# Kernel tuning notes

Measured on AMD Instinct MI355X. Metric: run time of the kernel, lower is better.

## Reference

```python
import jax, jax.numpy as jnp
import numpy as np

E = 512      # embed_dim
H = 8        # num_heads
D = E // H   # head_dim


def setup_inputs() -> dict:
    key = jax.random.key(0)
    ks = jax.random.split(key, 10)
    T, S, B = 2048, 2048, 4
    inp = {}
    inp["query_r"] = jax.random.normal(ks[0], (T, B, E), jnp.float32)
    inp["query_i"] = jax.random.normal(ks[1], (T, B, E), jnp.float32)
    inp["key_r"]   = jax.random.normal(ks[2], (S, B, E), jnp.float32)
    inp["key_i"]   = jax.random.normal(ks[3], (S, B, E), jnp.float32)
    inp["value_r"] = jax.random.normal(ks[4], (S, B, E), jnp.float32)
    inp["value_i"] = jax.random.normal(ks[5], (S, B, E), jnp.float32)
    # xavier-ish scale for complex weights (split real/imag)
    w_scale = 1.0 / np.sqrt(2.0 * E)
    inp["in_w_r"]  = jax.random.normal(ks[6], (3 * E, E), jnp.float32) * w_scale
    inp["in_w_i"]  = jax.random.normal(ks[7], (3 * E, E), jnp.float32) * w_scale
    inp["in_b_r"]  = jnp.zeros((3 * E,), jnp.float32)
    inp["in_b_i"]  = jnp.zeros((3 * E,), jnp.float32)
    inp["out_w_r"] = jax.random.normal(ks[8], (E, E), jnp.float32) * w_scale
    inp["out_w_i"] = jax.random.normal(ks[9], (E, E), jnp.float32) * w_scale
    inp["out_b_r"] = jnp.zeros((E,), jnp.float32)
    inp["out_b_i"] = jnp.zeros((E,), jnp.float32)
    return inp


def _clinear(xr, xi, wr, wi, br, bi):
    # complex linear: (xr + i xi) @ (wr + i wi)^T + (br + i bi)
    yr = xr @ wr.T - xi @ wi.T + br
    yi = xr @ wi.T + xi @ wr.T + bi
    return yr, yi


def reference(query_r, query_i, key_r, key_i, value_r, value_i,
              in_w_r, in_w_i, in_b_r, in_b_i,
              out_w_r, out_w_i, out_b_r, out_b_i):
    T, B, _ = query_r.shape
    S = key_r.shape[0]
    # in-projection (packed q/k/v rows of in_proj_weight)
    qr, qi = _clinear(query_r, query_i, in_w_r[:E], in_w_i[:E], in_b_r[:E], in_b_i[:E])
    kr, ki = _clinear(key_r, key_i, in_w_r[E:2*E], in_w_i[E:2*E], in_b_r[E:2*E], in_b_i[E:2*E])
    vr, vi = _clinear(value_r, value_i, in_w_r[2*E:], in_w_i[2*E:], in_b_r[2*E:], in_b_i[2*E:])
    # split heads: (T,B,E) -> (T,B,H,D)
    qr = qr.reshape(T, B, H, D); qi = qi.reshape(T, B, H, D)
    kr = kr.reshape(S, B, H, D); ki = ki.reshape(S, B, H, D)
    vr = vr.reshape(S, B, H, D); vi = vi.reshape(S, B, H, D)
    scale = 1.0 / np.sqrt(D).astype(np.float32)
    # Re[Q K^H] = Qr.Kr + Qi.Ki  (conjugate transpose cancels imag cross terms)
    scores = (jnp.einsum('tbhd,sbhd->bhts', qr, kr)
              + jnp.einsum('tbhd,sbhd->bhts', qi, ki)) * scale
    p = jax.nn.softmax(scores, axis=-1)          # (B,H,T,S) real
    # complex AV with real attention weights
    or_ = jnp.einsum('bhts,sbhd->tbhd', p, vr).reshape(T, B, E)
    oi_ = jnp.einsum('bhts,sbhd->tbhd', p, vi).reshape(T, B, E)
    # out-projection (complex linear)
    out_r, out_i = _clinear(or_, oi_, out_w_r, out_w_i, out_b_r, out_b_i)
    attn_weights = p.mean(axis=1)                # averaged over heads: (B,T,S)
    return out_r, out_i, attn_weights
```

## Files before the change

kernel.cpp:

```cpp
#include <hip/hip_runtime.h>


typedef _Float16 half8 __attribute__((ext_vector_type(8)));
typedef _Float16 half2v __attribute__((ext_vector_type(2)));
typedef float f32x4 __attribute__((ext_vector_type(4)));
typedef float f32x2 __attribute__((ext_vector_type(2)));
typedef unsigned uint2v __attribute__((ext_vector_type(2)));
typedef unsigned uint4v __attribute__((ext_vector_type(4)));

__device__ __forceinline__ f32x4 mfma16(half8 a, half8 b, f32x4 c) {
  return __builtin_amdgcn_mfma_f32_16x16x32_f16(a, b, c, 0, 0, 0);
}

__device__ __forceinline__ half8 cvt8(f32x4 a, f32x4 b) {
  half8 h;
  h[0] = (_Float16)a[0]; h[1] = (_Float16)a[1]; h[2] = (_Float16)a[2]; h[3] = (_Float16)a[3];
  h[4] = (_Float16)b[0]; h[5] = (_Float16)b[1]; h[6] = (_Float16)b[2]; h[7] = (_Float16)b[3];
  return h;
}

__device__ __forceinline__ half8 neg8(half8 a) {
  half8 r;
#pragma unroll
  for (int i = 0; i < 8; i++) r[i] = -a[i];
  return r;
}

__device__ __forceinline__ unsigned pkrtz(float a, float b) {
  return __builtin_bit_cast(unsigned, __builtin_amdgcn_cvt_pkrtz(a, b));
}

__device__ __forceinline__ float fexp2(float x) { return __builtin_amdgcn_exp2f(x); }

__device__ __forceinline__ void gload16(const void* g, void* l) {
  __builtin_amdgcn_global_load_lds((const __attribute__((address_space(1))) void*)g,
                                   (__attribute__((address_space(3))) void*)l, 16, 0, 0);
}

__global__ __launch_bounds__(256) void cvt_weights_kernel(
    const float* __restrict__ iwr, const float* __restrict__ iwi,
    const float* __restrict__ owr, const float* __restrict__ owi,
    _Float16* __restrict__ dst) {
  const int i = blockIdx.x * 256 + threadIdx.x;
  const float* src;
  long so, doff;
  if (i < 98304)       { src = iwr; so = (long)i * 8;            doff = so; }
  else if (i < 196608) { src = iwi; so = (long)(i - 98304) * 8;  doff = 786432 + so; }
  else if (i < 229376) { src = owr; so = (long)(i - 196608) * 8; doff = 1572864 + so; }
  else                 { src = owi; so = (long)(i - 229376) * 8; doff = 1835008 + so; }
  f32x4 a = *(const f32x4*)(src + so);
  f32x4 b = *(const f32x4*)(src + so + 4);
  *(half8*)(dst + doff) = cvt8(a, b);
}

__global__ __launch_bounds__(256, 2) void inproj_kernel(
    const float* __restrict__ xqr, const float* __restrict__ xqi,
    const float* __restrict__ xkr, const float* __restrict__ xki,
    const float* __restrict__ xvr, const float* __restrict__ xvi,
    const _Float16* __restrict__ wr, const _Float16* __restrict__ wi,
    const float* __restrict__ br_, const float* __restrict__ bi_,
    _Float16* __restrict__ qp, _Float16* __restrict__ kp,
    _Float16* __restrict__ vp) {
  __shared__ float As_r[4096], As_i[4096];
  __shared__ _Float16 Bs_r[4096], Bs_i[4096];
  const int proj = blockIdx.z;
  const float* xr = (proj == 0) ? xqr : (proj == 1) ? xkr : xvr;
  const float* xi = (proj == 0) ? xqi : (proj == 1) ? xki : xvi;
  const int lane = threadIdx.x & 63, wave = threadIdx.x >> 6;
  const int c = lane & 15, g = lane >> 4;
  const int wrow = (wave >> 1) * 64, wcol = (wave & 1) * 64;
  const int m0 = blockIdx.x * 128, n0 = blockIdx.y * 128;

  const int acol = ((lane & 7) ^ (lane >> 3)) * 4;
  const int bcol = ((lane & 3) ^ ((lane >> 3) & 3)) * 8;
  const int sa = (c & 7) << 2;
  const int sb = ((c >> 1) & 3) << 3;

  f32x4 accR[4][4] = {};
  f32x4 accI[4][4] = {};

#pragma unroll 1
  for (int kk = 0; kk < 512; kk += 32) {
#pragma unroll
    for (int q = 0; q < 4; q++) {
      const int grp = wave * 4 + q;
      const int arow = grp * 8 + (lane >> 3);
      const long go = (long)(m0 + arow) * 512 + kk + acol;
      gload16(xr + go, &As_r[grp * 256]);
      gload16(xi + go, &As_i[grp * 256]);
    }
#pragma unroll
    for (int q = 0; q < 2; q++) {
      const int grp = wave * 2 + q;
      const int brow = grp * 16 + (lane >> 2);
      const long go = (long)(proj * 512 + n0 + brow) * 512 + kk + bcol;
      gload16(wr + go, &Bs_r[grp * 512]);
      gload16(wi + go, &Bs_i[grp * 512]);
    }
    __syncthreads();
    half8 a_r[4], a_i[4], a_ni[4];
#pragma unroll
    for (int mt = 0; mt < 4; mt++) {
      const int arow = wrow + mt * 16 + c;
      f32x4 lo = *(const f32x4*)&As_r[arow * 32 + ((g * 8) ^ sa)];
      f32x4 hi = *(const f32x4*)&As_r[arow * 32 + ((g * 8 + 4) ^ sa)];
      a_r[mt] = cvt8(lo, hi);
      lo = *(const f32x4*)&As_i[arow * 32 + ((g * 8) ^ sa)];
      hi = *(const f32x4*)&As_i[arow * 32 + ((g * 8 + 4) ^ sa)];
      a_i[mt] = cvt8(lo, hi);
      a_ni[mt] = neg8(a_i[mt]);
    }
#pragma unroll
    for (int nt = 0; nt < 4; nt++) {
      const int brow = wcol + nt * 16 + c;
      const half8 bR = *(const half8*)&Bs_r[brow * 32 + ((g * 8) ^ sb)];
      const half8 bI = *(const half8*)&Bs_i[brow * 32 + ((g * 8) ^ sb)];
#pragma unroll
      for (int mt = 0; mt < 4; mt++) {
        accR[mt][nt] = mfma16(a_r[mt], bR, accR[mt][nt]);
        accR[mt][nt] = mfma16(a_ni[mt], bI, accR[mt][nt]);
        accI[mt][nt] = mfma16(a_r[mt], bI, accI[mt][nt]);
        accI[mt][nt] = mfma16(a_i[mt], bR, accI[mt][nt]);
      }
    }
    __syncthreads();
  }
#pragma unroll
  for (int nt = 0; nt < 4; nt++) {
    const int n = n0 + wcol + nt * 16 + c;
    const float vbr = br_[proj * 512 + n];
    const float vbi = bi_[proj * 512 + n];
    const int hh = n >> 6, dl = n & 63;
#pragma unroll
    for (int mt = 0; mt < 4; mt++)
#pragma unroll
      for (int r = 0; r < 4; r++) {
        const int m = m0 + wrow + mt * 16 + g * 4 + r;
        const float yr = accR[mt][nt][r] + vbr;
        const float yi = accI[mt][nt][r] + vbi;
        const int row = m >> 2, bb = m & 3;
        if (proj == 2) {
          const long o = ((long)((bb * 8 + hh) * 64 + (row >> 5)) << 12)
                       + ((long)(dl >> 4) << 10)
                       + ((((row >> 3) & 3) * 16 + (dl & 15)) * 8) + (row & 7);
          vp[o] = (_Float16)yr;
          vp[o + 512] = (_Float16)yi;
        } else {
          const long o = ((long)((bb * 8 + hh) * 128 + (row >> 4)) << 11)
                       + ((long)(dl >> 5) << 10)
                       + ((((dl >> 3) & 3) * 16 + (row & 15)) * 8) + (dl & 7);
          _Float16* dst = (proj == 0) ? qp : kp;
          dst[o] = (_Float16)yr;
          dst[o + 512] = (_Float16)yi;
        }
      }
  }
}

__device__ __forceinline__ void p1_load(half8 (&a)[8],
    const _Float16* kb, int s0) {
  const _Float16* p = kb + (long)(s0 >> 4) * 2048;
#pragma unroll
  for (int j = 0; j < 4; j++) {
    a[j]     = *(const half8*)(p + j * 512);
    a[4 + j] = *(const half8*)(p + 2048 + j * 512);
  }
}

__device__ __forceinline__ void p1_proc(const half8 (&a)[8], const half8 (&qf)[4],
                                        float& mrun, float& lrun) {
  const float SC2 = 0.18033688011112042f;
  f32x4 acc0 = {0.f, 0.f, 0.f, 0.f}, acc1 = {0.f, 0.f, 0.f, 0.f};
  __builtin_amdgcn_s_setprio(1);
  acc0 = mfma16(a[0], qf[0], acc0);
  acc0 = mfma16(a[1], qf[1], acc0);
  acc0 = mfma16(a[2], qf[2], acc0);
  acc0 = mfma16(a[3], qf[3], acc0);
  acc1 = mfma16(a[4], qf[0], acc1);
  acc1 = mfma16(a[5], qf[1], acc1);
  acc1 = mfma16(a[6], qf[2], acc1);
  acc1 = mfma16(a[7], qf[3], acc1);
  __builtin_amdgcn_s_setprio(0);
  float s2[8];
#pragma unroll
  for (int r = 0; r < 4; r++) { s2[r] = acc0[r] * SC2; s2[4 + r] = acc1[r] * SC2; }
  float tm = s2[0];
#pragma unroll
  for (int j = 1; j < 8; j++) tm = fmaxf(tm, s2[j]);
  const float nm = fmaxf(mrun, tm);
  float sum = 0.0f;
#pragma unroll
  for (int j = 0; j < 8; j++) sum += fexp2(s2[j] - nm);
  lrun = lrun * fexp2(mrun - nm) + sum;
  mrun = nm;
}

__global__ __launch_bounds__(256) void pass1_kernel(
    const _Float16* __restrict__ qp, const _Float16* __restrict__ kp,
    float* __restrict__ c_out) {
  const int lane = threadIdx.x & 63, wave = threadIdx.x >> 6;
  const int c = lane & 15;
  const int lin = blockIdx.x;
  const int h = lin & 7, b = (lin >> 3) & 3;
  const int t0 = (lin >> 5) * 64 + wave * 16;

  const _Float16* qb = qp + ((long)(b * 8 + h) * 128 + (t0 >> 4)) * 2048 + lane * 8;
  half8 qf[4];
#pragma unroll
  for (int j = 0; j < 4; j++) qf[j] = *(const half8*)(qb + j * 512);

  float mrun = -1e30f, lrun = 0.0f;
  const _Float16* kb = kp + (long)(b * 8 + h) * 262144 + lane * 8;

  half8 bufA[8], bufB[8];
  p1_load(bufA, kb, 0);
  p1_load(bufB, kb, 32);
#pragma unroll 1
  for (int s0 = 0; s0 < 2048; s0 += 64) {
    p1_proc(bufA, qf, mrun, lrun);
    p1_load(bufA, kb, (s0 + 64) & 2047);
    p1_proc(bufB, qf, mrun, lrun);
    p1_load(bufB, kb, (s0 + 96) & 2047);
  }
#pragma unroll
  for (int off = 16; off <= 32; off <<= 1) {
    const float mo = __shfl_xor(mrun, off, 64);
    const float lo = __shfl_xor(lrun, off, 64);
    const float nm = fmaxf(mrun, mo);
    lrun = lrun * fexp2(mrun - nm) + lo * fexp2(mo - nm);
    mrun = nm;
  }
  if (lane < 16) {
    const int idx = (b * 8 + h) * 2048 + t0 + c;
    c_out[idx] = -(mrun + __log2f(lrun));
  }
}

__device__ __forceinline__ void load_kswap(half8 (&kf)[8],
    const _Float16* kb, int s) {
  const _Float16* p = kb + (long)(s >> 4) * 2048;
#pragma unroll
  for (int j = 0; j < 4; j++) {
    kf[j]     = *(const half8*)(p + j * 512);
    kf[4 + j] = *(const half8*)(p + 2048 + j * 512);
  }
}

__device__ __forceinline__ void load_vv(half8 (&vf)[8],
    const _Float16* vb, int s) {
  const _Float16* p = vb + (long)(s >> 5) * 4096;
#pragma unroll
  for (int t = 0; t < 8; t++) vf[t] = *(const half8*)(p + t * 512);
}

__device__ __forceinline__ void p2_compute(
    int s0, _Float16* wbuf, half8 (&kf)[8], half8 (&vf)[8],
    const half8 (&qf)[8], float c0, float c1,
    f32x4 (&oacc)[2][4][2],
    const _Float16* kb, const _Float16* vb,
    int c, int g, int h) {
  const float SC2 = 0.18033688011112042f;
  f32x4 sacc[2][2];
  __builtin_amdgcn_s_setprio(1);
#pragma unroll
  for (int st = 0; st < 2; st++)
#pragma unroll
    for (int sq = 0; sq < 2; sq++) {
      f32x4 a = {0.f, 0.f, 0.f, 0.f};
      a = mfma16(kf[sq * 4 + 0], qf[st * 4 + 0], a);
      a = mfma16(kf[sq * 4 + 1], qf[st * 4 + 1], a);
      a = mfma16(kf[sq * 4 + 2], qf[st * 4 + 2], a);
      a = mfma16(kf[sq * 4 + 3], qf[st * 4 + 3], a);
      sacc[st][sq] = a;
    }
  __builtin_amdgcn_s_setprio(0);
  const int sn = (s0 + 32) & 2047;
  load_kswap(kf, kb, sn);
  half8 pa0, pa1;
#pragma unroll
  for (int st = 0; st < 2; st++) {
    const float cc = st ? c1 : c0;
    float p[8];
#pragma unroll
    for (int r = 0; r < 4; r++) {
      p[r]     = fexp2(fmaf(sacc[st][0][r], SC2, cc));
      p[4 + r] = fexp2(fmaf(sacc[st][1][r], SC2, cc));
    }
    const unsigned X0 = pkrtz(p[0], p[1]), X1 = pkrtz(p[2], p[3]);
    const unsigned Y0 = pkrtz(p[4], p[5]), Y1 = pkrtz(p[6], p[7]);
    const uint2v ab0 = __builtin_amdgcn_permlane32_swap(X0, Y0, false, false);
    const uint2v ab1 = __builtin_amdgcn_permlane32_swap(X1, Y1, false, false);
    const uint2v cd0 = __builtin_amdgcn_permlane16_swap(ab0[0], ab0[1], false, false);
    const uint2v cd1 = __builtin_amdgcn_permlane16_swap(ab1[0], ab1[1], false, false);
    uint4v u;
    u[0] = cd0[0]; u[1] = cd1[0]; u[2] = cd0[1]; u[3] = cd1[1];
    const half8 pav = __builtin_bit_cast(half8, u);
    if (st == 0) pa0 = pav; else pa1 = pav;
    *(half8*)(wbuf + (h * 32 + st * 16 + c) * 40 + g * 8) = pav;
  }
  __builtin_amdgcn_s_setprio(1);
#pragma unroll
  for (int dt = 0; dt < 4; dt++) {
    oacc[0][dt][0] = mfma16(pa0, vf[dt * 2 + 0], oacc[0][dt][0]);
    oacc[0][dt][1] = mfma16(pa0, vf[dt * 2 + 1], oacc[0][dt][1]);
    oacc[1][dt][0] = mfma16(pa1, vf[dt * 2 + 0], oacc[1][dt][0]);
    oacc[1][dt][1] = mfma16(pa1, vf[dt * 2 + 1], oacc[1][dt][1]);
  }
  __builtin_amdgcn_s_setprio(0);
  load_vv(vf, vb, sn);
}

__device__ __forceinline__ void p2_meanread(
    const _Float16* rbuf, int s_read, float* attn_base, int tid) {
  const _Float16* mp = rbuf + (tid >> 4) * 40 + (tid & 15) * 2;
  half2v s = *(const half2v*)(mp);
#pragma unroll
  for (int w = 1; w < 8; w++) s += *(const half2v*)(mp + w * 1280);
  f32x2 out2 = {(float)s[0] * 0.125f, (float)s[1] * 0.125f};
  *(f32x2*)(attn_base + s_read) = out2;
}

__global__ __launch_bounds__(512, 2) void pass2_kernel(
    const _Float16* __restrict__ qp, const _Float16* __restrict__ kp,
    const _Float16* __restrict__ vp,
    const float* __restrict__ c_in,
    _Float16* __restrict__ orh, _Float16* __restrict__ oih,
    float* __restrict__ attn) {
  __shared__ _Float16 plds[4][8][32][40];
  const int tid = threadIdx.x;
  const int lane = tid & 63, h = tid >> 6;
  const int c = lane & 15, g = lane >> 4;
  const int lin = blockIdx.x;
  const int b = (lin & 7) >> 1;
  const int t0 = (((lin & 1) << 5) | (lin >> 3)) * 32;

  const _Float16* qb = qp + ((long)(b * 8 + h) * 128 + (t0 >> 4)) * 2048 + lane * 8;
  half8 qf[8];
#pragma unroll
  for (int st = 0; st < 2; st++)
#pragma unroll
    for (int j = 0; j < 4; j++)
      qf[st * 4 + j] = *(const half8*)(qb + st * 2048 + j * 512);

  const int midx = (b * 8 + h) * 2048 + t0 + c;
  const float c0 = c_in[midx];
  const float c1 = c_in[midx + 16];

  f32x4 oacc[2][4][2] = {};
  const _Float16* kb = kp + (long)(b * 8 + h) * 262144 + lane * 8;
  const _Float16* vb = vp + (long)(b * 8 + h) * 262144 + lane * 8;
  float* attn_base = attn + ((long)b * 2048 + t0 + (tid >> 4)) * 2048 + (tid & 15) * 2;
  _Float16* pb0 = &plds[0][0][0][0];
  _Float16* pb1 = &plds[1][0][0][0];
  _Float16* pb2 = &plds[2][0][0][0];
  _Float16* pb3 = &plds[3][0][0][0];

  half8 kf[8], vf[8];
  load_kswap(kf, kb, 0);
  load_vv(vf, vb, 0);

#pragma unroll 1
  for (int s0 = 0; s0 < 2048; s0 += 128) {
    p2_compute(s0, pb0, kf, vf, qf, c0, c1, oacc, kb, vb, c, g, h);
    __syncthreads();
    if (s0 >= 32) p2_meanread(pb3, s0 - 32, attn_base, tid);
    p2_compute(s0 + 32, pb1, kf, vf, qf, c0, c1, oacc, kb, vb, c, g, h);
    __syncthreads();
    p2_meanread(pb0, s0, attn_base, tid);
    p2_compute(s0 + 64, pb2, kf, vf, qf, c0, c1, oacc, kb, vb, c, g, h);
    __syncthreads();
    p2_meanread(pb1, s0 + 32, attn_base, tid);
    p2_compute(s0 + 96, pb3, kf, vf, qf, c0, c1, oacc, kb, vb, c, g, h);
    __syncthreads();
    p2_meanread(pb2, s0 + 64, attn_base, tid);
  }
  p2_meanread(pb3, 2016, attn_base, tid);

#pragma unroll
  for (int st = 0; st < 2; st++)
#pragma unroll
    for (int dt = 0; dt < 4; dt++)
#pragma unroll
      for (int r = 0; r < 4; r++) {
        const int t = t0 + st * 16 + g * 4 + r;
        const long row = (long)(t * 4 + b) * 512 + h * 64 + dt * 16 + c;
        orh[row] = (_Float16)oacc[st][dt][0][r];
        oih[row] = (_Float16)oacc[st][dt][1][r];
      }
}

__global__ __launch_bounds__(256, 2) void outproj_kernel(
    const _Float16* __restrict__ xr, const _Float16* __restrict__ xi,
    const _Float16* __restrict__ wr, const _Float16* __restrict__ wi,
    const float* __restrict__ br_, const float* __restrict__ bi_,
    float* __restrict__ outr, float* __restrict__ outi) {
  __shared__ _Float16 As_r[4096], As_i[4096];
  __shared__ _Float16 Bs_r[4096], Bs_i[4096];
  const int lane = threadIdx.x & 63, wave = threadIdx.x >> 6;
  const int c = lane & 15, g = lane >> 4;
  const int wrow = (wave >> 1) * 64, wcol = (wave & 1) * 64;
  const int m0 = blockIdx.x * 128, n0 = blockIdx.y * 128;

  const int bcol = ((lane & 3) ^ ((lane >> 3) & 3)) * 8;
  const int sb = ((c >> 1) & 3) << 3;

  f32x4 accR[4][4] = {};
  f32x4 accI[4][4] = {};

#pragma unroll 1
  for (int kk = 0; kk < 512; kk += 32) {
#pragma unroll
    for (int q = 0; q < 2; q++) {
      const int grp = wave * 2 + q;
      const int row = grp * 16 + (lane >> 2);
      const long ga = (long)(m0 + row) * 512 + kk + bcol;
      const long gb = (long)(n0 + row) * 512 + kk + bcol;
      gload16(xr + ga, &As_r[grp * 512]);
      gload16(xi + ga, &As_i[grp * 512]);
      gload16(wr + gb, &Bs_r[grp * 512]);
      gload16(wi + gb, &Bs_i[grp * 512]);
    }
    __syncthreads();
    half8 a_r[4], a_i[4], a_ni[4];
#pragma unroll
    for (int mt = 0; mt < 4; mt++) {
      const int arow = wrow + mt * 16 + c;
      a_r[mt] = *(const half8*)&As_r[arow * 32 + ((g * 8) ^ sb)];
      a_i[mt] = *(const half8*)&As_i[arow * 32 + ((g * 8) ^ sb)];
      a_ni[mt] = neg8(a_i[mt]);
    }
#pragma unroll
    for (int nt = 0; nt < 4; nt++) {
      const int brow = wcol + nt * 16 + c;
      const half8 bR = *(const half8*)&Bs_r[brow * 32 + ((g * 8) ^ sb)];
      const half8 bI = *(const half8*)&Bs_i[brow * 32 + ((g * 8) ^ sb)];
#pragma unroll
      for (int mt = 0; mt < 4; mt++) {
        accR[mt][nt] = mfma16(a_r[mt], bR, accR[mt][nt]);
        accR[mt][nt] = mfma16(a_ni[mt], bI, accR[mt][nt]);
        accI[mt][nt] = mfma16(a_r[mt], bI, accI[mt][nt]);
        accI[mt][nt] = mfma16(a_i[mt], bR, accI[mt][nt]);
      }
    }
    __syncthreads();
  }
#pragma unroll
  for (int nt = 0; nt < 4; nt++) {
    const int n = n0 + wcol + nt * 16 + c;
    const float vbr = br_[n], vbi = bi_[n];
#pragma unroll
    for (int mt = 0; mt < 4; mt++)
#pragma unroll
      for (int r = 0; r < 4; r++) {
        const int m = m0 + wrow + mt * 16 + g * 4 + r;
        outr[(long)m * 512 + n] = accR[mt][nt][r] + vbr;
        outi[(long)m * 512 + n] = accI[mt][nt][r] + vbi;
      }
  }
}

extern "C" void kernel_launch(void* const* d_in, const int* in_sizes, int n_in,
                              void* d_out, int out_size, void* d_ws, size_t ws_size,
                              hipStream_t stream) {
  const float* query_r = (const float*)d_in[0];
  const float* query_i = (const float*)d_in[1];
  const float* key_r   = (const float*)d_in[2];
  const float* key_i   = (const float*)d_in[3];
  const float* value_r = (const float*)d_in[4];
  const float* value_i = (const float*)d_in[5];
  const float* in_w_r  = (const float*)d_in[6];
  const float* in_w_i  = (const float*)d_in[7];
  const float* in_b_r  = (const float*)d_in[8];
  const float* in_b_i  = (const float*)d_in[9];
  const float* out_w_r = (const float*)d_in[10];
  const float* out_w_i = (const float*)d_in[11];
  const float* out_b_r = (const float*)d_in[12];
  const float* out_b_i = (const float*)d_in[13];

  _Float16* ws = (_Float16*)d_ws;
  _Float16* w16_inr  = ws;
  _Float16* w16_ini  = ws + 786432;
  _Float16* w16_outr = ws + 1572864;
  _Float16* w16_outi = ws + 1835008;
  _Float16* Qp  = ws + 2097152;
  _Float16* Kp  = Qp + 8388608;
  _Float16* Vp  = Kp + 8388608;
  _Float16* orh = Vp + 8388608;
  _Float16* oih = orh + 4194304;
  float* c_arr = (float*)ws;

  float* outr = (float*)d_out;
  float* outi = outr + 4194304;
  float* attn = outr + 8388608;

  cvt_weights_kernel<<<1024, 256, 0, stream>>>(in_w_r, in_w_i, out_w_r, out_w_i, ws);

  inproj_kernel<<<dim3(64, 4, 3), 256, 0, stream>>>(
      query_r, query_i, key_r, key_i, value_r, value_i,
      w16_inr, w16_ini, in_b_r, in_b_i,
      Qp, Kp, Vp);

  pass1_kernel<<<1024, 256, 0, stream>>>(Qp, Kp, c_arr);

  pass2_kernel<<<256, 512, 0, stream>>>(
      Qp, Kp, Vp, c_arr, orh, oih, attn);

  outproj_kernel<<<dim3(64, 4), 256, 0, stream>>>(
      orh, oih, w16_outr, w16_outi, out_b_r, out_b_i, outr, outi);
}
```

Measured before the change: 284.0 us.

## Convert in-projection activations to fp16 in registers and widen pass1 blocks

New measurement: 272.9 us. 1.04x faster.

```diff
diff --git a/kernel.cpp b/kernel.cpp
--- a/kernel.cpp
+++ b/kernel.cpp
@@ -61,34 +61,48 @@
     const float* __restrict__ br_, const float* __restrict__ bi_,
     _Float16* __restrict__ qp, _Float16* __restrict__ kp,
     _Float16* __restrict__ vp) {
-  __shared__ float As_r[4096], As_i[4096];
+  __shared__ _Float16 As_r[4096], As_i[4096];
   __shared__ _Float16 Bs_r[4096], Bs_i[4096];
   const int proj = blockIdx.z;
   const float* xr = (proj == 0) ? xqr : (proj == 1) ? xkr : xvr;
   const float* xi = (proj == 0) ? xqi : (proj == 1) ? xki : xvi;
-  const int lane = threadIdx.x & 63, wave = threadIdx.x >> 6;
+  const int tid = threadIdx.x;
+  const int lane = tid & 63, wave = tid >> 6;
   const int c = lane & 15, g = lane >> 4;
   const int wrow = (wave >> 1) * 64, wcol = (wave & 1) * 64;
   const int m0 = blockIdx.x * 128, n0 = blockIdx.y * 128;
 
-  const int acol = ((lane & 7) ^ (lane >> 3)) * 4;
+  const int ar = tid >> 1;
+  const int acg = (tid & 1) * 2;
+  const int aswz = (ar >> 1) & 3;
+  const float* xr_st = xr + (long)(m0 + ar) * 512 + acg * 8;
+  const float* xi_st = xi + (long)(m0 + ar) * 512 + acg * 8;
+  _Float16* aw_r0 = &As_r[ar * 32 + ((acg ^ aswz) << 3)];
+  _Float16* aw_r1 = &As_r[ar * 32 + (((acg + 1) ^ aswz) << 3)];
+  _Float16* aw_i0 = &As_i[ar * 32 + ((acg ^ aswz) << 3)];
+  _Float16* aw_i1 = &As_i[ar * 32 + (((acg + 1) ^ aswz) << 3)];
+
   const int bcol = ((lane & 3) ^ ((lane >> 3) & 3)) * 8;
-  const int sa = (c & 7) << 2;
   const int sb = ((c >> 1) & 3) << 3;
 
   f32x4 accR[4][4] = {};
   f32x4 accI[4][4] = {};
 
+  f32x4 r0 = *(const f32x4*)(xr_st);
+  f32x4 r1 = *(const f32x4*)(xr_st + 4);
+  f32x4 r2 = *(const f32x4*)(xr_st + 8);
+  f32x4 r3 = *(const f32x4*)(xr_st + 12);
+  f32x4 i0 = *(const f32x4*)(xi_st);
+  f32x4 i1 = *(const f32x4*)(xi_st + 4);
+  f32x4 i2 = *(const f32x4*)(xi_st + 8);
+  f32x4 i3 = *(const f32x4*)(xi_st + 12);
+
 #pragma unroll 1
   for (int kk = 0; kk < 512; kk += 32) {
-#pragma unroll
-    for (int q = 0; q < 4; q++) {
-      const int grp = wave * 4 + q;
-      const int arow = grp * 8 + (lane >> 3);
-      const long go = (long)(m0 + arow) * 512 + kk + acol;
-      gload16(xr + go, &As_r[grp * 256]);
-      gload16(xi + go, &As_i[grp * 256]);
-    }
+    *(half8*)aw_r0 = cvt8(r0, r1);
+    *(half8*)aw_r1 = cvt8(r2, r3);
+    *(half8*)aw_i0 = cvt8(i0, i1);
+    *(half8*)aw_i1 = cvt8(i2, i3);
 #pragma unroll
     for (int q = 0; q < 2; q++) {
       const int grp = wave * 2 + q;
@@ -98,16 +112,22 @@
       gload16(wi + go, &Bs_i[grp * 512]);
     }
     __syncthreads();
+    if (kk < 480) {
+      r0 = *(const f32x4*)(xr_st + kk + 32);
+      r1 = *(const f32x4*)(xr_st + kk + 36);
+      r2 = *(const f32x4*)(xr_st + kk + 40);
+      r3 = *(const f32x4*)(xr_st + kk + 44);
+      i0 = *(const f32x4*)(xi_st + kk + 32);
+      i1 = *(const f32x4*)(xi_st + kk + 36);
+      i2 = *(const f32x4*)(xi_st + kk + 40);
+      i3 = *(const f32x4*)(xi_st + kk + 44);
+    }
     half8 a_r[4], a_i[4], a_ni[4];
 #pragma unroll
     for (int mt = 0; mt < 4; mt++) {
       const int arow = wrow + mt * 16 + c;
-      f32x4 lo = *(const f32x4*)&As_r[arow * 32 + ((g * 8) ^ sa)];
-      f32x4 hi = *(const f32x4*)&As_r[arow * 32 + ((g * 8 + 4) ^ sa)];
-      a_r[mt] = cvt8(lo, hi);
-      lo = *(const f32x4*)&As_i[arow * 32 + ((g * 8) ^ sa)];
-      hi = *(const f32x4*)&As_i[arow * 32 + ((g * 8 + 4) ^ sa)];
-      a_i[mt] = cvt8(lo, hi);
+      a_r[mt] = *(const half8*)&As_r[arow * 32 + ((g * 8) ^ sb)];
+      a_i[mt] = *(const half8*)&As_i[arow * 32 + ((g * 8) ^ sb)];
       a_ni[mt] = neg8(a_i[mt]);
     }
 #pragma unroll
@@ -195,14 +215,14 @@
   mrun = nm;
 }
 
-__global__ __launch_bounds__(256) void pass1_kernel(
+__global__ __launch_bounds__(512) void pass1_kernel(
     const _Float16* __restrict__ qp, const _Float16* __restrict__ kp,
     float* __restrict__ c_out) {
   const int lane = threadIdx.x & 63, wave = threadIdx.x >> 6;
   const int c = lane & 15;
   const int lin = blockIdx.x;
   const int h = lin & 7, b = (lin >> 3) & 3;
-  const int t0 = (lin >> 5) * 64 + wave * 16;
+  const int t0 = (lin >> 5) * 128 + wave * 16;
 
   const _Float16* qb = qp + ((long)(b * 8 + h) * 128 + (t0 >> 4)) * 2048 + lane * 8;
   half8 qf[4];
@@ -500,7 +520,7 @@
       w16_inr, w16_ini, in_b_r, in_b_i,
       Qp, Kp, Vp);
 
-  pass1_kernel<<<1024, 256, 0, stream>>>(Qp, Kp, c_arr);
+  pass1_kernel<<<512, 512, 0, stream>>>(Qp, Kp, c_arr);
 
   pass2_kernel<<<256, 512, 0, stream>>>(
       Qp, Kp, Vp, c_arr, orh, oih, attn);
```
